# Kernel tuning notes

Hardware: AMD Instinct MI355X
Metric: run time of the kernel (lower is better)

Reference implementation:

```python
import jax, jax.numpy as jnp
import numpy as np

B, T, D = 4, 4000, 1024
H = 8
DK = D // H          # key dim per head; value dim per head also DK (value_factor=1)
CHUNK = 500
EPS_LN = 1e-5
EPS_RMS = 1e-6


def rotate_every_two(x):
    x1 = x[..., ::2]
    x2 = x[..., 1::2]
    return jnp.stack((-x2, x1), axis=-1).reshape(x.shape)


def theta_shift(x, sin, cos):
    # x: [b,h,t,dk]; sin/cos: [t,dk]
    return x * cos + rotate_every_two(x) * sin


def rel_pos(slen, chunk_len, num_heads, key_dim):
    # RetNetRelPos(chunkwise_recurrent=True)
    angle = 1.0 / (10000 ** jnp.linspace(0.0, 1.0, key_dim // 2))
    angle = jnp.repeat(angle, 2)  # == unsqueeze(-1).repeat(1,2).flatten()
    decay = jnp.log(1.0 - 2.0 ** (-5.0 - jnp.arange(num_heads, dtype=jnp.float32)))
    index = jnp.arange(slen, dtype=jnp.float32)
    sin = jnp.sin(index[:, None] * angle[None, :])  # [t,dk]
    cos = jnp.cos(index[:, None] * angle[None, :])
    bi = jnp.arange(chunk_len, dtype=jnp.float32)
    tril = jnp.tril(jnp.ones((chunk_len, chunk_len), bool))
    diff = bi[:, None] - bi[None, :]
    mask = jnp.where(tril[None], jnp.exp(decay[:, None, None] * diff[None]), 0.0)  # [H,C,C]
    last_row = mask[:, -1]                                            # [H,C]
    value_inner_decay = (last_row / last_row.sum(-1, keepdims=True))[:, :, None]  # [H,C,1]
    scale = jnp.sqrt(mask.sum(-1, keepdims=True))                     # [H,C,1]
    inner_mask = mask / scale
    cross_decay = jnp.exp(decay * chunk_len)[:, None, None]           # [H,1,1]
    qid = jnp.exp(decay[:, None] * (bi + 1.0))[:, :, None]            # [H,C,1]
    query_inner_decay = qid / (scale / last_row.sum(-1)[:, None, None])
    return (sin, cos), (inner_mask, cross_decay, query_inner_decay, value_inner_decay)


def retention_chunkwise(qr, kr, v, inner):
    mask, cross_decay, query_inner_decay, value_inner_decay = inner
    b, t = v.shape[0], v.shape[1]
    C = mask.shape[1]
    n = t // C
    h, dk = qr.shape[1], qr.shape[3]
    dv = v.shape[2] // h
    # [b,h,t,dk] -> [b,n,h,C,dk]
    qr = qr.transpose(0, 2, 1, 3).reshape(b, n, C, h, dk).transpose(0, 1, 3, 2, 4)
    kr = kr.transpose(0, 2, 1, 3).reshape(b, n, C, h, dk).transpose(0, 1, 3, 2, 4)
    v = v.reshape(b, n, C, h, dv).transpose(0, 1, 3, 2, 4)  # [b,n,h,C,dv]

    qk = jnp.einsum('bnhcd,bnhed->bnhce', qr, kr) * mask  # [b,n,h,C,C]
    inner_scale = jnp.clip(jnp.abs(jax.lax.stop_gradient(qk)).sum(-1, keepdims=True), 1.0, None)
    qk = qk / inner_scale
    inner_output = jnp.einsum('bnhce,bnhed->bnhcd', qk, v)  # [b,n,h,C,dv]

    kv = jnp.einsum('bnhck,bnhcv->bnhkv', kr, v * value_inner_decay)  # [b,n,h,dk,dv]

    def step(carry, kv_i):
        kv_state, kv_scale = carry
        out = (kv_state / kv_scale, kv_scale)
        new_state = kv_state * cross_decay + kv_i
        sg = jnp.abs(jax.lax.stop_gradient(new_state)).sum(-2, keepdims=True).max(-1, keepdims=True)
        return (new_state, jnp.clip(sg, 1.0, None)), out

    init = (jnp.zeros((b, h, dk, dv), v.dtype), jnp.ones((b, h, 1, 1), v.dtype))
    _, (kv_rec, cross_scale) = jax.lax.scan(step, init, jnp.moveaxis(kv, 1, 0))
    kv_rec = jnp.moveaxis(kv_rec, 0, 1)            # [b,n,h,dk,dv]
    cross_scale = jnp.moveaxis(cross_scale, 0, 1)  # [b,n,h,1,1]

    all_scale = jnp.maximum(inner_scale, cross_scale)
    cross_output = jnp.einsum('bnhcd,bnhdv->bnhcv', qr * query_inner_decay, kv_rec)
    output = inner_output / (all_scale / inner_scale) + cross_output / (all_scale / cross_scale)
    return output.transpose(0, 1, 3, 2, 4).reshape(b, t, h, dv)  # [b,t,h,dv]


def setup_inputs() -> dict:
    key = jax.random.key(0)
    ks = jax.random.split(key, 6)
    s = 0.02
    return {
        'inputs': jax.random.normal(ks[0], (B, T, D), jnp.float32),
        'ln_gamma': jnp.ones((D,), jnp.float32),
        'ln_beta': jnp.zeros((D,), jnp.float32),
        'Wq': jax.random.normal(ks[1], (D, D), jnp.float32) * s,
        'Wk': jax.random.normal(ks[2], (D, D), jnp.float32) * s,
        'Wv': jax.random.normal(ks[3], (D, D), jnp.float32) * s,
        'Wg': jax.random.normal(ks[4], (D, D), jnp.float32) * s,
        'Wo': jax.random.normal(ks[5], (D, D), jnp.float32) * s,
    }


def reference(inputs, ln_gamma, ln_beta, Wq, Wk, Wv, Wg, Wo):
    b, t, d = inputs.shape
    # pre-LayerNorm
    mu = inputs.mean(-1, keepdims=True)
    var = ((inputs - mu) ** 2).mean(-1, keepdims=True)
    x = (inputs - mu) / jnp.sqrt(var + EPS_LN) * ln_gamma + ln_beta

    (sin, cos), inner = rel_pos(t, CHUNK, H, DK)

    q = (x @ Wq).reshape(b, t, H, DK).transpose(0, 2, 1, 3)
    k = (x @ Wk * (DK ** -0.5)).reshape(b, t, H, DK).transpose(0, 2, 1, 3)
    v = x @ Wv
    g = x @ Wg

    qr = theta_shift(q, sin, cos)
    kr = theta_shift(k, sin, cos)

    out = retention_chunkwise(qr, kr, v, inner)  # [b,t,H,dv]
    # group norm: per-head RMSNorm without affine
    out = out * jax.lax.rsqrt(jnp.mean(out ** 2, -1, keepdims=True) + EPS_RMS)
    out = out.reshape(b, t, H * DK)
    out = jax.nn.silu(g) * out
    return out @ Wo  # dropout is identity in eval
```

## Files before the change

kernel.cpp:

```cpp
#include <hip/hip_runtime.h>
#include <hip/hip_bf16.h>


typedef __attribute__((ext_vector_type(4))) float f32x4;
typedef __attribute__((ext_vector_type(8))) short s16x8;

#define DEV static __device__ __forceinline__

DEV float bfu(ushort u){ union{uint i; float f;} x; x.i=((uint)u)<<16; return x.f; }
DEV float bflo(uint w){ union{uint i; float f;} x; x.i=w<<16; return x.f; }
DEV float bfhi(uint w){ union{uint i; float f;} x; x.i=w&0xffff0000u; return x.f; }
DEV ushort f2bf(float f){ union{float f; uint u;} x; x.f=f; uint r = x.u + 0x7fffu + ((x.u>>16)&1u); return (ushort)(r>>16); }
DEV uint pack2(float lo, float hi){ return ((uint)f2bf(hi)<<16) | (uint)f2bf(lo); }

DEV void gload16(const ushort* g, ushort* l) {
  __builtin_amdgcn_global_load_lds((const __attribute__((address_space(1))) void*)g,
                                   (__attribute__((address_space(3))) void*)l, 16, 0, 0);
}

__global__ __launch_bounds__(256) void f2bf_t_all(const float* __restrict__ s0, const float* __restrict__ s1,
                                                  const float* __restrict__ s2, const float* __restrict__ s3,
                                                  const float* __restrict__ s4,
                                                  ushort* __restrict__ d0, ushort* __restrict__ d1,
                                                  ushort* __restrict__ d2, ushort* __restrict__ d3,
                                                  ushort* __restrict__ d4) {
  const float* src; ushort* dst;
  switch (blockIdx.z) {
    case 0: src=s0; dst=d0; break;
    case 1: src=s1; dst=d1; break;
    case 2: src=s2; dst=d2; break;
    case 3: src=s3; dst=d3; break;
    default: src=s4; dst=d4; break;
  }
  __shared__ ushort t[64][72];
  int kt = blockIdx.x*64, nt = blockIdx.y*64;
  int tid = threadIdx.x;
  int r = tid>>2, c0 = (tid&3)*16;
  const float* s = src + (size_t)(kt+r)*1024 + nt + c0;
  #pragma unroll
  for (int j=0;j<16;j+=4) {
    float4 vv = *(const float4*)(s+j);
    t[r][c0+j]=f2bf(vv.x); t[r][c0+j+1]=f2bf(vv.y); t[r][c0+j+2]=f2bf(vv.z); t[r][c0+j+3]=f2bf(vv.w);
  }
  __syncthreads();
  union { uint4 u4[2]; ushort s16[16]; } tmp;
  #pragma unroll
  for (int j=0;j<16;j++) tmp.s16[j] = t[c0+j][r];
  ushort* d = dst + (size_t)(nt+r)*1024 + kt + c0;
  *(uint4*)(d)   = tmp.u4[0];
  *(uint4*)(d+8) = tmp.u4[1];
}

__global__ __launch_bounds__(256) void ln_kernel(const float* __restrict__ x,
                                                 const float* __restrict__ gamma,
                                                 const float* __restrict__ beta,
                                                 ushort* __restrict__ xo) {
  int row = blockIdx.x;
  int tid = threadIdx.x;
  const float* xr = x + (size_t)row*1024;
  float4 u = ((const float4*)xr)[tid];
  float s = u.x+u.y+u.z+u.w;
  float sq = u.x*u.x+u.y*u.y+u.z*u.z+u.w*u.w;
  #pragma unroll
  for (int o=32;o;o>>=1){ s += __shfl_xor(s,o); sq += __shfl_xor(sq,o); }
  __shared__ float red[8];
  int wv=tid>>6, ln=tid&63;
  if (ln==0){ red[wv]=s; red[4+wv]=sq; }
  __syncthreads();
  s = red[0]+red[1]+red[2]+red[3];
  sq = red[4]+red[5]+red[6]+red[7];
  float mu = s*(1.0f/1024.0f);
  float var = sq*(1.0f/1024.0f)-mu*mu;
  float inv = rsqrtf(var+1e-5f);
  float4 gg = ((const float4*)gamma)[tid];
  float4 bb = ((const float4*)beta)[tid];
  float o0=(u.x-mu)*inv*gg.x+bb.x;
  float o1=(u.y-mu)*inv*gg.y+bb.y;
  float o2=(u.z-mu)*inv*gg.z+bb.z;
  float o3=(u.w-mu)*inv*gg.w+bb.w;
  uint2 w; w.x=pack2(o0,o1); w.y=pack2(o2,o3);
  ((uint2*)(xo+(size_t)row*1024))[tid]=w;
}

__global__ __launch_bounds__(256) void sincos_kernel(uint* __restrict__ cstab) {
  int idx = blockIdx.x*256+threadIdx.x;
  if (idx >= 4000*64) return;
  int t = idx>>6, i = idx&63;
  float ang = expf(-9.210340371976184f * (float)i * (1.0f/63.0f));
  float a = (float)t * ang;
  float sv = sinf(a), cv = cosf(a);
  uint p = pack2(cv, sv);
  cstab[(size_t)t*128+2*i]   = p;
  cstab[(size_t)t*128+2*i+1] = p;
}

__global__ __launch_bounds__(256) void gemm_proj(const ushort* __restrict__ A,
                                                 const ushort* __restrict__ BT,
                                                 ushort* __restrict__ qb,
                                                 ushort* __restrict__ kb,
                                                 ushort* __restrict__ gb,
                                                 ushort* __restrict__ kT,
                                                 ushort* __restrict__ vT,
                                                 const uint* __restrict__ cstab) {
  __attribute__((aligned(16))) __shared__ char smem[34816];
  ushort* As = (ushort*)smem;
  ushort* Bs = (ushort*)(smem+16384);
  const int K = 1024;
  int wg = blockIdx.x;
  int s, r9, sm;
  if (wg < 3584) { s = wg>>9; r9 = wg&511; sm = 16; }
  else           { s = 7;     r9 = wg-3584; sm = 13; }
  int nblk = r9 / sm;
  int mloc = r9 - nblk*sm;
  int bm = (s*16 + mloc)*128, bn = nblk*128;
  int tid = threadIdx.x;
  int w = tid>>6, l = tid&63;
  int wm = (w>>1)*64, wn = (w&1)*64;
  int rsel = l&15, ko = (l>>4)*8;
  f32x4 acc[4][4];
  #pragma unroll
  for (int a2=0;a2<4;a2++)
    #pragma unroll
    for (int j=0;j<4;j++){ acc[a2][j][0]=0; acc[a2][j][1]=0; acc[a2][j][2]=0; acc[a2][j][3]=0; }
  const ushort* ap0 = A  + (size_t)(bm + w*32 + (l>>2))*K + (l&3)*8;
  const ushort* ap1 = ap0 + (size_t)16*K;
  const ushort* bp0 = BT + (size_t)(bn + w*32 + (l>>2))*K + (l&3)*8;
  const ushort* bp1 = bp0 + (size_t)16*K;
  {
    ushort* ab = As + w*1024; ushort* bb2 = Bs + w*1024;
    gload16(ap0, ab); gload16(ap1, ab+512);
    gload16(bp0, bb2); gload16(bp1, bb2+512);
  }
  int cur = 0;
  for (int kt=0; kt<K; kt+=32) {
    __syncthreads();
    if (kt+32 < K) {
      int nb = cur^1;
      ushort* ab = As + nb*4096 + w*1024; ushort* bb2 = Bs + nb*4096 + w*1024;
      gload16(ap0+kt+32, ab); gload16(ap1+kt+32, ab+512);
      gload16(bp0+kt+32, bb2); gload16(bp1+kt+32, bb2+512);
    }
    const ushort* Ac = As + cur*4096;
    const ushort* Bc = Bs + cur*4096;
    s16x8 af[4], bfr[4];
    #pragma unroll
    for (int mf=0;mf<4;mf++) af[mf]  = *(const s16x8*)&Ac[(wm+mf*16+rsel)*32 + ko];
    #pragma unroll
    for (int nf=0;nf<4;nf++) bfr[nf] = *(const s16x8*)&Bc[(wn+nf*16+rsel)*32 + ko];
    #pragma unroll
    for (int mf=0;mf<4;mf++)
      #pragma unroll
      for (int nf=0;nf<4;nf++)
        acc[mf][nf] = __builtin_amdgcn_mfma_f32_16x16x32_bf16(af[mf], bfr[nf], acc[mf][nf], 0,0,0);
    cur ^= 1;
  }
  int proj = bn>>10;
  int bnp  = bn&1023;
  int hh   = bnp>>7;
  __syncthreads();
  ushort* Ct = (ushort*)smem;
  if (proj < 2) {
    float decay = logf(1.0f - exp2f(-5.0f-(float)hh));
    float ksc = 0.08838834764831845f;
    #pragma unroll
    for (int mf=0;mf<4;mf++) {
      #pragma unroll
      for (int r2=0;r2<4;r2++) {
        int rowt = wm+mf*16+(l>>4)*4+r2;
        int grow = bm+rowt;
        int t = grow - (grow/4000)*4000;
        int cch = t - (t/500)*500;
        float esc = (proj==0)? expf(decay*(float)cch) : expf(-decay*(float)cch)*ksc;
        const uint* cst = cstab + (size_t)t*128;
        #pragma unroll
        for (int nf=0;nf<4;nf++) {
          int colt = wn+nf*16+(l&15);
          float vv = acc[mf][nf][r2];
          uint wcs = cst[colt];
          float cc = bflo(wcs), ss = bfhi(wcs);
          float ov = __shfl_xor(vv,1);
          float rot = ((l&1)==0)? (vv*cc-ov*ss) : (vv*cc+ov*ss);
          Ct[rowt*136+colt] = f2bf(rot*esc);
        }
      }
    }
  } else {
    #pragma unroll
    for (int mf=0;mf<4;mf++)
      #pragma unroll
      for (int nf=0;nf<4;nf++) {
        int colt = wn+nf*16+(l&15);
        #pragma unroll
        for (int r2=0;r2<4;r2++)
          Ct[(wm+mf*16+(l>>4)*4+r2)*136+colt] = f2bf(acc[mf][nf][r2]);
      }
  }
  __syncthreads();
  if (proj != 2) {
    ushort* dst = (proj==0)? qb : (proj==1)? kb : gb;
    int r = tid>>1, ch=(tid&1)*64;
    ushort* drow = dst + (size_t)(bm+r)*1024 + bnp + ch;
    #pragma unroll
    for (int j=0;j<8;j++) *(uint4*)(drow+j*8) = *(uint4*)&Ct[r*136+ch+j*8];
  }
  if (proj==1 || proj==2) {
    ushort* Tdst = (proj==1)? kT : vT;
    int dloc = tid>>1, rh=(tid&1)*64;
    #pragma unroll
    for (int j=0;j<8;j++) {
      int gr = bm + rh + j*8;
      int bb = gr/4000; int t0 = gr - bb*4000;
      int ch0 = t0/500; int c0 = t0 - ch0*500;
      if (c0 <= 492) {
        union{uint4 u; ushort s[8];} pk;
        #pragma unroll
        for (int ii=0;ii<8;ii++) pk.s[ii] = Ct[(rh+j*8+ii)*136 + dloc];
        *(uint4*)(Tdst + ((size_t)(bb*64+ch0*8+hh))*65536 + (size_t)dloc*512 + c0) = pk.u;
      } else {
        #pragma unroll
        for (int ii=0;ii<8;ii++) {
          int gri = gr+ii; int bbi=gri/4000; int ti=gri-bbi*4000; int chi=ti/500; int ci=ti-chi*500;
          Tdst[((size_t)(bbi*64+chi*8+hh))*65536 + (size_t)dloc*512 + ci] = Ct[(rh+j*8+ii)*136+dloc];
        }
      }
    }
  }
}

__global__ __launch_bounds__(256) void gemm_out(const ushort* __restrict__ A,
                                                const ushort* __restrict__ BT,
                                                float* __restrict__ C) {
  __attribute__((aligned(16))) __shared__ char smem[34816];
  ushort* As = (ushort*)smem;
  ushort* Bs = (ushort*)(smem+16384);
  const int K = 1024;
  int wg = blockIdx.x;
  int s, r9, sm;
  if (wg < 896) { s = wg>>7; r9 = wg&127; sm = 16; }
  else          { s = 7;     r9 = wg-896; sm = 13; }
  int nblk = r9 / sm;
  int mloc = r9 - nblk*sm;
  int bm = (s*16 + mloc)*128, bn = nblk*128;
  int tid = threadIdx.x;
  int w = tid>>6, l = tid&63;
  int wm = (w>>1)*64, wn = (w&1)*64;
  int rsel = l&15, ko = (l>>4)*8;
  f32x4 acc[4][4];
  #pragma unroll
  for (int a2=0;a2<4;a2++)
    #pragma unroll
    for (int j=0;j<4;j++){ acc[a2][j][0]=0; acc[a2][j][1]=0; acc[a2][j][2]=0; acc[a2][j][3]=0; }
  const ushort* ap0 = A  + (size_t)(bm + w*32 + (l>>2))*K + (l&3)*8;
  const ushort* ap1 = ap0 + (size_t)16*K;
  const ushort* bp0 = BT + (size_t)(bn + w*32 + (l>>2))*K + (l&3)*8;
  const ushort* bp1 = bp0 + (size_t)16*K;
  {
    ushort* ab = As + w*1024; ushort* bb2 = Bs + w*1024;
    gload16(ap0, ab); gload16(ap1, ab+512);
    gload16(bp0, bb2); gload16(bp1, bb2+512);
  }
  int cur = 0;
  for (int kt=0; kt<K; kt+=32) {
    __syncthreads();
    if (kt+32 < K) {
      int nb = cur^1;
      ushort* ab = As + nb*4096 + w*1024; ushort* bb2 = Bs + nb*4096 + w*1024;
      gload16(ap0+kt+32, ab); gload16(ap1+kt+32, ab+512);
      gload16(bp0+kt+32, bb2); gload16(bp1+kt+32, bb2+512);
    }
    const ushort* Ac = As + cur*4096;
    const ushort* Bc = Bs + cur*4096;
    s16x8 af[4], bfr[4];
    #pragma unroll
    for (int mf=0;mf<4;mf++) af[mf]  = *(const s16x8*)&Ac[(wm+mf*16+rsel)*32 + ko];
    #pragma unroll
    for (int nf=0;nf<4;nf++) bfr[nf] = *(const s16x8*)&Bc[(wn+nf*16+rsel)*32 + ko];
    #pragma unroll
    for (int mf=0;mf<4;mf++)
      #pragma unroll
      for (int nf=0;nf<4;nf++)
        acc[mf][nf] = __builtin_amdgcn_mfma_f32_16x16x32_bf16(af[mf], bfr[nf], acc[mf][nf], 0,0,0);
    cur ^= 1;
  }
  __syncthreads();
  float* Cf = (float*)smem;
  #pragma unroll
  for (int half=0; half<2; half++) {
    if ((w>>1)==half) {
      #pragma unroll
      for (int mf=0;mf<4;mf++)
        #pragma unroll
        for (int nf=0;nf<4;nf++)
          #pragma unroll
          for (int r2=0;r2<4;r2++)
            Cf[(mf*16+(l>>4)*4+r2)*132 + wn+nf*16+(l&15)] = acc[mf][nf][r2];
    }
    __syncthreads();
    {
      int r = tid>>2, cs=(tid&3)*32;
      float* drow = C + (size_t)(bm+half*64+r)*1024 + bn + cs;
      #pragma unroll
      for (int j=0;j<8;j++) *(float4*)(drow+j*4) = *(float4*)&Cf[r*132+cs+j*4];
    }
    __syncthreads();
  }
}

__global__ __launch_bounds__(256) void kv_mfma(const ushort* __restrict__ kT,
                                               const ushort* __restrict__ vT,
                                               float* __restrict__ kvp) {
  int bnh = blockIdx.x;
  __shared__ ushort sh2[16384];
  int tid=threadIdx.x;
  int wv=tid>>6, l=tid&63, g=l>>4, c16=l&15;
  int wr = wv>>1, wc = wv&1;
  int ri[4], ro[4];
  #pragma unroll
  for (int jj=0;jj<4;jj++){
    int i = wv*256 + jj*64 + l;
    ri[jj] = i>>3;
    ro[jj] = (((i&7)*16) ^ ((ri[jj]&7)<<4))>>1;
  }
  const ushort* kbase = kT + (size_t)bnh*65536;
  const ushort* vbase = vT + (size_t)bnh*65536;
  f32x4 acc[4][4];
  #pragma unroll
  for (int i=0;i<4;i++)
    #pragma unroll
    for (int j=0;j<4;j++){ acc[i][j][0]=0; acc[i][j][1]=0; acc[i][j][2]=0; acc[i][j][3]=0; }
  for (int ctep=0; ctep<8; ctep++) {
    int cb = ctep*64;
    __syncthreads();
    #pragma unroll
    for (int jj=0;jj<4;jj++){
      gload16(kbase + (size_t)ri[jj]*512 + cb + ro[jj], (ushort*)((char*)sh2 + wv*4096 + jj*1024));
      gload16(vbase + (size_t)ri[jj]*512 + cb + ro[jj], (ushort*)((char*)sh2 + 16384 + wv*4096 + jj*1024));
    }
    __syncthreads();
    if (ctep==7) {
      for (int z=tid; z<128*12; z+=256) {
        int r = z/12, j = 52 + (z - (z/12)*12);
        *(ushort*)((char*)sh2 + 16384 + r*128 + ((j*2) ^ ((r&7)<<4))) = 0;
      }
      __syncthreads();
    }
    #pragma unroll
    for (int kc=0;kc<2;kc++) {
      s16x8 af[4], bf2[4];
      #pragma unroll
      for (int mf=0;mf<4;mf++){
        int row = wr*64+mf*16+c16;
        af[mf] = *(const s16x8*)((const char*)sh2 + row*128 + ((((kc*32+g*8)*2)) ^ ((row&7)<<4)));
      }
      #pragma unroll
      for (int nf=0;nf<4;nf++){
        int row = wc*64+nf*16+c16;
        bf2[nf] = *(const s16x8*)((const char*)sh2 + 16384 + row*128 + ((((kc*32+g*8)*2)) ^ ((row&7)<<4)));
      }
      #pragma unroll
      for (int mf=0;mf<4;mf++)
        #pragma unroll
        for (int nf=0;nf<4;nf++)
          acc[mf][nf] = __builtin_amdgcn_mfma_f32_16x16x32_bf16(af[mf], bf2[nf], acc[mf][nf], 0,0,0);
    }
  }
  float* outp = kvp + (size_t)bnh*16384;
  #pragma unroll
  for (int mf=0;mf<4;mf++)
    #pragma unroll
    for (int nf=0;nf<4;nf++)
      #pragma unroll
      for (int reg=0;reg<4;reg++)
        outp[(size_t)(wr*64+mf*16+g*4+reg)*128 + wc*64+nf*16+c16] = acc[mf][nf][reg];
}

__global__ __launch_bounds__(512) void scan_kernel(const float* __restrict__ kvp,
                                                   ushort* __restrict__ kvrecT,
                                                   float* __restrict__ crosssc) {
  int bh = blockIdx.x;
  int b = bh>>3, h = bh&7;
  float Dh = 1.0f - exp2f(-5.0f-(float)h);
  float decay = logf(Dh);
  float cd = expf(decay*500.0f);
  float ls = (1.0f - expf(decay*500.0f))/(1.0f-Dh);
  float cst = expf(decay*499.0f)/ls;
  int tid=threadIdx.x;
  int vcol = tid&127, kq = tid>>7;
  float st[32];
  #pragma unroll
  for (int i=0;i<32;i++) st[i]=0;
  float scale = 1.0f;
  __shared__ float colpart[4][128];
  __shared__ float sred[2];
  for (int n=0;n<8;n++) {
    int bnh = (b*8+n)*8+h;
    const float* src = kvp + (size_t)bnh*16384;
    ushort* rec = kvrecT + (size_t)bnh*16384;
    float inv = 1.0f/scale;
    float cs = 0;
    #pragma unroll
    for (int i=0;i<32;i++) {
      int kk = kq*32+i;
      rec[(size_t)vcol*128+kk] = f2bf(st[i]*inv);
      st[i] = st[i]*cd + cst*src[(size_t)kk*128+vcol];
      cs += fabsf(st[i]);
    }
    if (tid==0) crosssc[bnh] = scale;
    colpart[kq][vcol] = cs;
    __syncthreads();
    if (tid<128) colpart[0][tid] += colpart[1][tid] + colpart[2][tid] + colpart[3][tid];
    __syncthreads();
    float m = (tid<128)? colpart[0][tid] : 0.0f;
    #pragma unroll
    for (int o=32;o;o>>=1) m = fmaxf(m,__shfl_xor(m,o));
    if (tid<128 && (tid&63)==0) sred[tid>>6]=m;
    __syncthreads();
    scale = fmaxf(fmaxf(sred[0],sred[1]),1.0f);
    __syncthreads();
  }
}

__global__ __launch_bounds__(256,4) void iout_mfma(const ushort* __restrict__ qr,
                                                   const ushort* __restrict__ kr,
                                                   const ushort* __restrict__ vT,
                                                   const ushort* __restrict__ kvrecT,
                                                   const float* __restrict__ crosssc,
                                                   const ushort* __restrict__ gbuf,
                                                   ushort* __restrict__ opre) {
  int ib = blockIdx.x;
  int x = ib&7, u = ib>>3;
  int rt = u&7;
  int bnh = x*32 + (u>>3);
  int h = bnh&7, n=(bnh>>3)&7, b=bnh>>6;
  size_t base = (size_t)(b*4000+n*500)*1024 + h*128;
  float Dh = 1.0f - exp2f(-5.0f-(float)h);
  float decay = logf(Dh);
  __shared__ ushort sh[20480];
  char* shb = (char*)sh;
  int tid = threadIdx.x;
  int wv = tid>>6, l = tid&63;
  int g = l>>4, c16 = l&15;
  int r_base = rt*64 + wv*16 + g*4;

  int qrow = rt*64 + wv*16 + c16; if (qrow>499) qrow=499;
  s16x8 aq[4];
  #pragma unroll
  for (int kc=0;kc<4;kc++)
    aq[kc] = *(const s16x8*)(qr + base + (size_t)qrow*1024 + kc*32 + g*8);

  int ktrow[4], ktofs[4], vtrow[4], vtofs[4];
  #pragma unroll
  for (int jj=0;jj<4;jj++){
    int i = wv*256 + jj*64 + l;
    int r_ = i>>4;  ktrow[jj]=r_;  ktofs[jj] = (((i&15)*16) ^ ((r_&7)<<4))>>1;
    int r2_ = i>>3; vtrow[jj]=r2_; vtofs[jj] = (((i&7)*16) ^ ((r2_&7)<<4))>>1;
  }
  const ushort* vTb = vT + (size_t)bnh*65536;

  f32x4 pv[8], cc[8];
  #pragma unroll
  for (int i=0;i<8;i++){
    #pragma unroll
    for (int j=0;j<4;j++){ pv[i][j]=0.0f; cc[i][j]=0.0f; }
  }
  float rowsum[4] = {0,0,0,0};

  for (int et=0; et<=rt; et++) {
    __syncthreads();
    #pragma unroll
    for (int jj=0;jj<4;jj++){
      int gr = et*64 + ktrow[jj]; if (gr>499) gr=499;
      gload16(kr + base + (size_t)gr*1024 + ktofs[jj], (ushort*)(shb + wv*4096 + jj*1024));
      gload16(vTb + (size_t)vtrow[jj]*512 + et*64 + vtofs[jj], (ushort*)(shb + 16384 + wv*4096 + jj*1024));
    }
    __syncthreads();
    f32x4 S[4];
    #pragma unroll
    for (int i=0;i<4;i++){ S[i][0]=0; S[i][1]=0; S[i][2]=0; S[i][3]=0; }
    __builtin_amdgcn_s_setprio(1);
    #pragma unroll
    for (int kc=0;kc<4;kc++) {
      #pragma unroll
      for (int ni=0;ni<4;ni++) {
        int krow = ni*16+c16;
        s16x8 bf = *(const s16x8*)(shb + krow*256 + ((((kc*32+g*8)*2)) ^ ((krow&7)<<4)));
        S[ni] = __builtin_amdgcn_mfma_f32_16x16x32_bf16(aq[kc], bf, S[ni], 0,0,0);
      }
    }
    __builtin_amdgcn_s_setprio(0);
    bool diag = (et==rt);
    #pragma unroll
    for (int ni=0;ni<4;ni++) {
      int e_rel = et*64 + ni*16 + c16;
      #pragma unroll
      for (int reg=0;reg<4;reg++) {
        float p = S[ni][reg];
        if (diag && e_rel > r_base+reg) p = 0.0f;
        rowsum[reg] += fabsf(p);
        int prow = wv*16 + g*4 + reg;
        *(ushort*)(shb + 32768 + prow*128 + (((ni*16+c16)*2) ^ ((prow&7)<<4))) = f2bf(p);
      }
    }
    __builtin_amdgcn_s_setprio(1);
    #pragma unroll
    for (int kc=0;kc<2;kc++) {
      int prow = wv*16 + c16;
      s16x8 pa = *(const s16x8*)(shb + 32768 + prow*128 + ((((kc*32+g*8)*2)) ^ ((prow&7)<<4)));
      #pragma unroll
      for (int nf=0;nf<8;nf++) {
        int vrow = nf*16+c16;
        s16x8 vb = *(const s16x8*)(shb + 16384 + vrow*128 + ((((kc*32+g*8)*2)) ^ ((vrow&7)<<4)));
        pv[nf] = __builtin_amdgcn_mfma_f32_16x16x32_bf16(pa, vb, pv[nf], 0,0,0);
      }
    }
    __builtin_amdgcn_s_setprio(0);
  }
  #pragma unroll
  for (int reg=0;reg<4;reg++) {
    float s = rowsum[reg];
    s += __shfl_xor(s,1); s += __shfl_xor(s,2); s += __shfl_xor(s,4); s += __shfl_xor(s,8);
    rowsum[reg] = s;
  }
  __syncthreads();
  #pragma unroll
  for (int jj=0;jj<8;jj++){
    int i = wv*512 + jj*64 + l;
    int r_ = i>>4;
    int ofs = (((i&15)*16) ^ ((r_&7)<<4))>>1;
    gload16(kvrecT + (size_t)bnh*16384 + (size_t)r_*128 + ofs, (ushort*)(shb + wv*8192 + jj*1024));
  }
  __syncthreads();
  __builtin_amdgcn_s_setprio(1);
  #pragma unroll
  for (int kc=0;kc<4;kc++) {
    #pragma unroll
    for (int nf=0;nf<8;nf++) {
      int krow = nf*16+c16;
      s16x8 bb = *(const s16x8*)(shb + krow*256 + ((((kc*32+g*8)*2)) ^ ((krow&7)<<4)));
      cc[nf] = __builtin_amdgcn_mfma_f32_16x16x32_bf16(aq[kc], bb, cc[nf], 0,0,0);
    }
  }
  __builtin_amdgcn_s_setprio(0);
  float cs = crosssc[bnh];
  float lsum = (1.0f-expf(decay*500.0f))/(1.0f-Dh);
  float ed = expf(decay);
  #pragma unroll
  for (int reg=0;reg<4;reg++) {
    int rr = r_base + reg;
    if (rr < 500) {
      float rs = (1.0f-expf(decay*(float)(rr+1)))/(1.0f-Dh);
      float rsr = rsqrtf(rs);
      float is = fmaxf(1.0f, rowsum[reg]*rsr);
      float all = fmaxf(is, cs);
      float qid = ed*lsum*rsr;
      float fi = rsr/all;
      float fc = qid*(cs/all);
      float o[8]; float ssq = 0.0f;
      #pragma unroll
      for (int nf=0;nf<8;nf++){ o[nf] = pv[nf][reg]*fi + cc[nf][reg]*fc; ssq += o[nf]*o[nf]; }
      ssq += __shfl_xor(ssq,1); ssq += __shfl_xor(ssq,2); ssq += __shfl_xor(ssq,4); ssq += __shfl_xor(ssq,8);
      float rmss = rsqrtf(ssq*(1.0f/128.0f)+1e-6f);
      size_t rowoff = (size_t)(b*4000+n*500+rr)*1024 + h*128;
      #pragma unroll
      for (int nf=0;nf<8;nf++){
        float gv = bfu(gbuf[rowoff + nf*16 + c16]);
        float sg = gv/(1.0f+expf(-gv));
        opre[rowoff + nf*16 + c16] = f2bf(sg*o[nf]*rmss);
      }
    }
  }
}

extern "C" void kernel_launch(void* const* d_in, const int* in_sizes, int n_in,
                              void* d_out, int out_size, void* d_ws, size_t ws_size,
                              hipStream_t stream) {
  const float* x     = (const float*)d_in[0];
  const float* gamma = (const float*)d_in[1];
  const float* beta  = (const float*)d_in[2];
  const float* Wq    = (const float*)d_in[3];
  const float* Wk    = (const float*)d_in[4];
  const float* Wv    = (const float*)d_in[5];
  const float* Wg    = (const float*)d_in[6];
  const float* Wo    = (const float*)d_in[7];
  float* out = (float*)d_out;

  char* ws = (char*)d_ws;
  size_t off = 0;
  auto alloc = [&](size_t bytes)->void* { void* p = ws+off; off += (bytes+255)&~(size_t)255; return p; };
  const size_t BT1024 = (size_t)16000*1024;
  ushort* xln  = (ushort*)alloc(BT1024*2);
  ushort* q    = (ushort*)alloc(BT1024*2);
  ushort* k    = (ushort*)alloc(BT1024*2);
  ushort* g    = (ushort*)alloc(BT1024*2);
  ushort* WqT  = (ushort*)alloc((size_t)1024*1024*2);
  ushort* WkT  = (ushort*)alloc((size_t)1024*1024*2);
  ushort* WvT  = (ushort*)alloc((size_t)1024*1024*2);
  ushort* WgT  = (ushort*)alloc((size_t)1024*1024*2);
  ushort* WoT  = (ushort*)alloc((size_t)1024*1024*2);
  uint* cstab  = (uint*)alloc((size_t)4000*128*4);
  ushort* kT   = (ushort*)alloc((size_t)256*65536*2);
  ushort* vT   = (ushort*)alloc((size_t)256*65536*2);
  ushort* kvrecT=(ushort*)alloc((size_t)256*16384*2);
  float* crosssc = (float*)alloc(256*4);
  (void)ws_size; (void)in_sizes; (void)n_in; (void)out_size;

  ln_kernel<<<16000,256,0,stream>>>(x,gamma,beta,xln);
  sincos_kernel<<<1000,256,0,stream>>>(cstab);
  dim3 tt(16,16,5);
  f2bf_t_all<<<tt,256,0,stream>>>(Wq,Wk,Wv,Wg,Wo, WqT,WkT,WvT,WgT,WoT);

  gemm_proj<<<4000,256,0,stream>>>(xln, WqT, q, k, g, kT, vT, cstab);

  float* kvp = (float*)xln;
  kv_mfma<<<256,256,0,stream>>>(kT,vT,kvp);
  scan_kernel<<<32,512,0,stream>>>(kvp,kvrecT,crosssc);

  ushort* opre = xln;
  iout_mfma<<<2048,256,0,stream>>>(q,k,vT,kvrecT,crosssc,g,opre);

  gemm_out<<<1000,256,0,stream>>>(opre,WoT,out);
}
```

Before: 394.7 us.

## Merge prep kernels into one launch and split kv_mfma over two chunk halves

The LayerNorm, sin/cos table and weight transpose-convert kernels become one launch, with the block index picking the job. kv_mfma now splits the chunk reduction over two halves via a second grid dimension, which doubles its block count from 256 to 512 so more of the GPU is busy. Each half writes partial KV sums to a new dedicated fp32 buffer, and scan_kernel adds the two partials. This costs extra workspace and extra partial-sum traffic in exchange for fewer launches and more parallelism.

```diff
diff --git a/kernel.cpp b/kernel.cpp
--- a/kernel.cpp
+++ b/kernel.cpp
@@ -18,80 +18,80 @@
                                    (__attribute__((address_space(3))) void*)l, 16, 0, 0);
 }
 
-__global__ __launch_bounds__(256) void f2bf_t_all(const float* __restrict__ s0, const float* __restrict__ s1,
-                                                  const float* __restrict__ s2, const float* __restrict__ s3,
-                                                  const float* __restrict__ s4,
-                                                  ushort* __restrict__ d0, ushort* __restrict__ d1,
-                                                  ushort* __restrict__ d2, ushort* __restrict__ d3,
-                                                  ushort* __restrict__ d4) {
-  const float* src; ushort* dst;
-  switch (blockIdx.z) {
-    case 0: src=s0; dst=d0; break;
-    case 1: src=s1; dst=d1; break;
-    case 2: src=s2; dst=d2; break;
-    case 3: src=s3; dst=d3; break;
-    default: src=s4; dst=d4; break;
-  }
-  __shared__ ushort t[64][72];
-  int kt = blockIdx.x*64, nt = blockIdx.y*64;
+__global__ __launch_bounds__(256) void prep_kernel(
+    const float* __restrict__ x, const float* __restrict__ gamma, const float* __restrict__ beta,
+    ushort* __restrict__ xo, uint* __restrict__ cstab,
+    const float* __restrict__ s0, const float* __restrict__ s1, const float* __restrict__ s2,
+    const float* __restrict__ s3, const float* __restrict__ s4,
+    ushort* __restrict__ d0, ushort* __restrict__ d1, ushort* __restrict__ d2,
+    ushort* __restrict__ d3, ushort* __restrict__ d4) {
+  __attribute__((aligned(16))) __shared__ char pbuf[9216];
+  int bid = blockIdx.x;
   int tid = threadIdx.x;
-  int r = tid>>2, c0 = (tid&3)*16;
-  const float* s = src + (size_t)(kt+r)*1024 + nt + c0;
-  #pragma unroll
-  for (int j=0;j<16;j+=4) {
-    float4 vv = *(const float4*)(s+j);
-    t[r][c0+j]=f2bf(vv.x); t[r][c0+j+1]=f2bf(vv.y); t[r][c0+j+2]=f2bf(vv.z); t[r][c0+j+3]=f2bf(vv.w);
-  }
-  __syncthreads();
-  union { uint4 u4[2]; ushort s16[16]; } tmp;
-  #pragma unroll
-  for (int j=0;j<16;j++) tmp.s16[j] = t[c0+j][r];
-  ushort* d = dst + (size_t)(nt+r)*1024 + kt + c0;
-  *(uint4*)(d)   = tmp.u4[0];
-  *(uint4*)(d+8) = tmp.u4[1];
-}
-
-__global__ __launch_bounds__(256) void ln_kernel(const float* __restrict__ x,
-                                                 const float* __restrict__ gamma,
-                                                 const float* __restrict__ beta,
-                                                 ushort* __restrict__ xo) {
-  int row = blockIdx.x;
-  int tid = threadIdx.x;
-  const float* xr = x + (size_t)row*1024;
-  float4 u = ((const float4*)xr)[tid];
-  float s = u.x+u.y+u.z+u.w;
-  float sq = u.x*u.x+u.y*u.y+u.z*u.z+u.w*u.w;
-  #pragma unroll
-  for (int o=32;o;o>>=1){ s += __shfl_xor(s,o); sq += __shfl_xor(sq,o); }
-  __shared__ float red[8];
-  int wv=tid>>6, ln=tid&63;
-  if (ln==0){ red[wv]=s; red[4+wv]=sq; }
-  __syncthreads();
-  s = red[0]+red[1]+red[2]+red[3];
-  sq = red[4]+red[5]+red[6]+red[7];
-  float mu = s*(1.0f/1024.0f);
-  float var = sq*(1.0f/1024.0f)-mu*mu;
-  float inv = rsqrtf(var+1e-5f);
-  float4 gg = ((const float4*)gamma)[tid];
-  float4 bb = ((const float4*)beta)[tid];
-  float o0=(u.x-mu)*inv*gg.x+bb.x;
-  float o1=(u.y-mu)*inv*gg.y+bb.y;
-  float o2=(u.z-mu)*inv*gg.z+bb.z;
-  float o3=(u.w-mu)*inv*gg.w+bb.w;
-  uint2 w; w.x=pack2(o0,o1); w.y=pack2(o2,o3);
-  ((uint2*)(xo+(size_t)row*1024))[tid]=w;
-}
-
-__global__ __launch_bounds__(256) void sincos_kernel(uint* __restrict__ cstab) {
-  int idx = blockIdx.x*256+threadIdx.x;
-  if (idx >= 4000*64) return;
-  int t = idx>>6, i = idx&63;
-  float ang = expf(-9.210340371976184f * (float)i * (1.0f/63.0f));
-  float a = (float)t * ang;
-  float sv = sinf(a), cv = cosf(a);
-  uint p = pack2(cv, sv);
-  cstab[(size_t)t*128+2*i]   = p;
-  cstab[(size_t)t*128+2*i+1] = p;
+  if (bid < 16000) {
+    float* red = (float*)pbuf;
+    int row = bid;
+    const float* xr = x + (size_t)row*1024;
+    float4 u = ((const float4*)xr)[tid];
+    float s = u.x+u.y+u.z+u.w;
+    float sq = u.x*u.x+u.y*u.y+u.z*u.z+u.w*u.w;
+    #pragma unroll
+    for (int o=32;o;o>>=1){ s += __shfl_xor(s,o); sq += __shfl_xor(sq,o); }
+    int wv=tid>>6, ln=tid&63;
+    if (ln==0){ red[wv]=s; red[4+wv]=sq; }
+    __syncthreads();
+    s = red[0]+red[1]+red[2]+red[3];
+    sq = red[4]+red[5]+red[6]+red[7];
+    float mu = s*(1.0f/1024.0f);
+    float var = sq*(1.0f/1024.0f)-mu*mu;
+    float inv = rsqrtf(var+1e-5f);
+    float4 gg = ((const float4*)gamma)[tid];
+    float4 bb = ((const float4*)beta)[tid];
+    float o0=(u.x-mu)*inv*gg.x+bb.x;
+    float o1=(u.y-mu)*inv*gg.y+bb.y;
+    float o2=(u.z-mu)*inv*gg.z+bb.z;
+    float o3=(u.w-mu)*inv*gg.w+bb.w;
+    uint2 w; w.x=pack2(o0,o1); w.y=pack2(o2,o3);
+    ((uint2*)(xo+(size_t)row*1024))[tid]=w;
+  } else if (bid < 17000) {
+    int idx = (bid-16000)*256 + tid;
+    if (idx < 4000*64) {
+      int t = idx>>6, i = idx&63;
+      float ang = expf(-9.210340371976184f * (float)i * (1.0f/63.0f));
+      float a = (float)t * ang;
+      float sv = sinf(a), cv = cosf(a);
+      uint p = pack2(cv, sv);
+      cstab[(size_t)t*128+2*i]   = p;
+      cstab[(size_t)t*128+2*i+1] = p;
+    }
+  } else {
+    int fid = bid - 17000;
+    const float* src; ushort* dst;
+    switch (fid >> 8) {
+      case 0: src=s0; dst=d0; break;
+      case 1: src=s1; dst=d1; break;
+      case 2: src=s2; dst=d2; break;
+      case 3: src=s3; dst=d3; break;
+      default: src=s4; dst=d4; break;
+    }
+    int rem = fid & 255;
+    int kt = (rem&15)*64, nt = (rem>>4)*64;
+    ushort (*t)[72] = (ushort(*)[72])pbuf;
+    int r = tid>>2, c0 = (tid&3)*16;
+    const float* s = src + (size_t)(kt+r)*1024 + nt + c0;
+    #pragma unroll
+    for (int j=0;j<16;j+=4) {
+      float4 vv = *(const float4*)(s+j);
+      t[r][c0+j]=f2bf(vv.x); t[r][c0+j+1]=f2bf(vv.y); t[r][c0+j+2]=f2bf(vv.z); t[r][c0+j+3]=f2bf(vv.w);
+    }
+    __syncthreads();
+    union { uint4 u4[2]; ushort s16[16]; } tmp;
+    #pragma unroll
+    for (int j=0;j<16;j++) tmp.s16[j] = t[c0+j][r];
+    ushort* d = dst + (size_t)(nt+r)*1024 + kt + c0;
+    *(uint4*)(d)   = tmp.u4[0];
+    *(uint4*)(d+8) = tmp.u4[1];
+  }
 }
 
 __global__ __launch_bounds__(256) void gemm_proj(const ushort* __restrict__ A,
@@ -310,6 +310,7 @@
                                                const ushort* __restrict__ vT,
                                                float* __restrict__ kvp) {
   int bnh = blockIdx.x;
+  int half = blockIdx.y;
   __shared__ ushort sh2[16384];
   int tid=threadIdx.x;
   int wv=tid>>6, l=tid&63, g=l>>4, c16=l&15;
@@ -328,7 +329,7 @@
   for (int i=0;i<4;i++)
     #pragma unroll
     for (int j=0;j<4;j++){ acc[i][j][0]=0; acc[i][j][1]=0; acc[i][j][2]=0; acc[i][j][3]=0; }
-  for (int ctep=0; ctep<8; ctep++) {
+  for (int ctep=half*4; ctep<half*4+4; ctep++) {
     int cb = ctep*64;
     __syncthreads();
     #pragma unroll
@@ -364,7 +365,7 @@
           acc[mf][nf] = __builtin_amdgcn_mfma_f32_16x16x32_bf16(af[mf], bf2[nf], acc[mf][nf], 0,0,0);
     }
   }
-  float* outp = kvp + (size_t)bnh*16384;
+  float* outp = kvp + ((size_t)half*256 + bnh)*16384;
   #pragma unroll
   for (int mf=0;mf<4;mf++)
     #pragma unroll
@@ -394,7 +395,8 @@
   __shared__ float sred[2];
   for (int n=0;n<8;n++) {
     int bnh = (b*8+n)*8+h;
-    const float* src = kvp + (size_t)bnh*16384;
+    const float* src0 = kvp + (size_t)bnh*16384;
+    const float* src1 = kvp + (size_t)(256+bnh)*16384;
     ushort* rec = kvrecT + (size_t)bnh*16384;
     float inv = 1.0f/scale;
     float cs = 0;
@@ -402,7 +404,7 @@
     for (int i=0;i<32;i++) {
       int kk = kq*32+i;
       rec[(size_t)vcol*128+kk] = f2bf(st[i]*inv);
-      st[i] = st[i]*cd + cst*src[(size_t)kk*128+vcol];
+      st[i] = st[i]*cd + cst*(src0[(size_t)kk*128+vcol] + src1[(size_t)kk*128+vcol]);
       cs += fabsf(st[i]);
     }
     if (tid==0) crosssc[bnh] = scale;
@@ -601,18 +603,17 @@
   ushort* kT   = (ushort*)alloc((size_t)256*65536*2);
   ushort* vT   = (ushort*)alloc((size_t)256*65536*2);
   ushort* kvrecT=(ushort*)alloc((size_t)256*16384*2);
+  float* kvp   = (float*)alloc((size_t)512*16384*4);
   float* crosssc = (float*)alloc(256*4);
   (void)ws_size; (void)in_sizes; (void)n_in; (void)out_size;
 
-  ln_kernel<<<16000,256,0,stream>>>(x,gamma,beta,xln);
-  sincos_kernel<<<1000,256,0,stream>>>(cstab);
-  dim3 tt(16,16,5);
-  f2bf_t_all<<<tt,256,0,stream>>>(Wq,Wk,Wv,Wg,Wo, WqT,WkT,WvT,WgT,WoT);
+  prep_kernel<<<18280,256,0,stream>>>(x,gamma,beta,xln,cstab,
+                                      Wq,Wk,Wv,Wg,Wo, WqT,WkT,WvT,WgT,WoT);
 
   gemm_proj<<<4000,256,0,stream>>>(xln, WqT, q, k, g, kT, vT, cstab);
 
-  float* kvp = (float*)xln;
-  kv_mfma<<<256,256,0,stream>>>(kT,vT,kvp);
+  dim3 gkv(256,2);
+  kv_mfma<<<gkv,256,0,stream>>>(kT,vT,kvp);
   scan_kernel<<<32,512,0,stream>>>(kvp,kvrecT,crosssc);
 
   ushort* opre = xln;
```

Measured after the change: 399.9 us. Within noise of the previous version (+1.3%).
